# Optimization experiments

Hardware: AMD Instinct MI355X
Metric: run time of the kernel (lower is better)

The kernel has to match this reference:

```python
import jax, jax.numpy as jnp
import numpy as np

# (dv=3, dc=6)-regular Tanner graph: M checks, N=2M vars, E=M*dc edges
M, N, DV, DC, D, B, T = 1024, 2048, 3, 6, 8, 128, 5
CIN = DC * D          # check-MLP in/out dim = 48
VIN = DV * D + 1      # var-MLP in/out dim  = 25 (extra scalar = LLR)
HC, HV = 4 * CIN, 4 * VIN
EPS = 1e-6


def _graph():
    # variable j connects to checks (j + l) % M, l = 0..DV-1 -> every check has degree DC
    var_nbrs = (np.arange(N)[:, None] + np.arange(DV)[None, :]) % M   # [N, DV] check ids
    # var-edge id e = j*DV + l ; sort edges by check to get check-slot ordering
    order = np.argsort(var_nbrs.reshape(-1), kind='stable')           # check-edge p -> var-edge e
    chk_nbrs = (order // DV).reshape(M, DC)                           # var id in each check slot
    inv_order = np.argsort(order)                                     # var-edge e -> check-edge p
    return chk_nbrs, order, inv_order


def setup_inputs() -> dict:
    key = jax.random.key(0)
    ks = jax.random.split(key, 12)
    chk_nbrs, order, inv_order = _graph()
    prior = np.clip(np.random.default_rng(0).uniform(0.005, 0.05, size=N), EPS, 1 - EPS)
    prior_llr = jnp.asarray(np.log((1.0 - prior) / prior), jnp.float32)

    def lin_w(k, g, nin, nout):
        return jax.random.normal(k, (g, nin, nout), jnp.float32) / np.sqrt(nin)

    def lin_b(k, g, nout):
        return 0.02 * jax.random.normal(k, (g, nout), jnp.float32)

    return {
        "syndromes": jax.random.randint(ks[0], (B, M), 0, 2, jnp.int32),
        "prior_llr": prior_llr,
        "chk_w1": lin_w(ks[1], M, CIN, HC), "chk_b1": lin_b(ks[2], M, HC),
        "chk_w2": lin_w(ks[3], M, HC, CIN), "chk_b2": lin_b(ks[4], M, CIN),
        "var_w1": lin_w(ks[5], N, VIN, HV), "var_b1": lin_b(ks[6], N, HV),
        "var_w2": lin_w(ks[7], N, HV, VIN), "var_b2": lin_b(ks[8], N, VIN),
        "chk_nbrs": jnp.asarray(chk_nbrs, jnp.int32),      # [M, DC] var id per check slot
        "c2v_gather": jnp.asarray(inv_order, jnp.int32),   # var-edge -> check-edge perm
        "v2c_gather": jnp.asarray(order, jnp.int32),       # check-edge -> var-edge perm
    }


def reference(syndromes, prior_llr, chk_w1, chk_b1, chk_w2, chk_b2,
              var_w1, var_b1, var_w2, var_b2, chk_nbrs, c2v_gather, v2c_gather):
    synd_sgn = (1 - 2 * syndromes).astype(jnp.float32)                    # [B, M]
    prior_b = jnp.broadcast_to(prior_llr, (B, N))[..., None]              # [B, N, 1]

    def chk_mlp(x):  # x: [B, M, CIN], per-check grouped GEMM
        h = jax.nn.gelu(jnp.einsum('bmi,mih->bmh', x, chk_w1) + chk_b1, approximate=False)
        return jnp.einsum('bmh,mho->bmo', h, chk_w2) + chk_b2

    def var_mlp(x):  # x: [B, N, VIN]
        h = jax.nn.gelu(jnp.einsum('bni,nih->bnh', x, var_w1) + var_b1, approximate=False)
        return jnp.einsum('bnh,nho->bno', h, var_w2) + var_b2

    # init check in-messages: zeros with first component = prior LLR of neighbor var
    chk_in = jnp.zeros((B, M, DC, D), jnp.float32).at[..., 0].set(prior_llr[chk_nbrs][None])

    def step(chk_in, _):
        y = chk_mlp(chk_in.reshape(B, M, CIN)).reshape(B, M, DC, D)
        y = y * synd_sgn[:, :, None, None]                                # syndrome sign flip
        var_in = y.reshape(B, M * DC, D)[:, c2v_gather]                   # scatter c->v as gather
        x = jnp.concatenate([var_in.reshape(B, N, DV * D), prior_b], axis=-1)
        out = var_mlp(x)
        llr = out[..., DV * D]                                            # [B, N]
        msg = out[..., :DV * D].reshape(B, N * DV, D)
        chk_in_new = msg[:, v2c_gather].reshape(B, M, DC, D)              # scatter v->c as gather
        return chk_in_new, llr

    _, llrs = jax.lax.scan(step, chk_in, None, length=T)
    return llrs  # [T, B, N]
```

## Files before the change

kernel.cpp:

```cpp
#include <hip/hip_runtime.h>
#include <math.h>

#define MM 1024
#define NN 2048
#define BB 128
#define TT 5
#define EE 6144

typedef __bf16 bf16x8 __attribute__((ext_vector_type(8)));
typedef __bf16 bf16x4 __attribute__((ext_vector_type(4)));
typedef short  s16x4  __attribute__((ext_vector_type(4)));
typedef float  f32x4  __attribute__((ext_vector_type(4)));
typedef unsigned int u32x4 __attribute__((ext_vector_type(4)));

typedef const __attribute__((address_space(1))) void* gas_p;
typedef __attribute__((address_space(3))) void* las_p;

#define CHK_W_ELEMS 22272
#define CHK_L2_OFF  12288
#define VAR_W_ELEMS 7168
#define VAR_L2_OFF  3584

__device__ __forceinline__ float gelu_fast(float x) {
    float xe = x * 0.70710678118654752f;
    float ax = fabsf(xe);
    float t  = __builtin_amdgcn_rcpf(1.0f + 0.3275911f * ax);
    float p  = t * (0.254829592f + t * (-0.284496736f + t * (1.421413741f +
               t * (-1.453152027f + t * 1.061405429f))));
    float er = 1.0f - p * __expf(-xe * xe);
    er = copysignf(er, xe);
    return 0.5f * x * (1.0f + er);
}

__device__ __forceinline__ f32x4 mfma16(bf16x4 a, bf16x4 b, f32x4 c) {
#if __has_builtin(__builtin_amdgcn_mfma_f32_16x16x16bf16_1k)
    return __builtin_amdgcn_mfma_f32_16x16x16bf16_1k(
        __builtin_bit_cast(s16x4, a), __builtin_bit_cast(s16x4, b), c, 0, 0, 0);
#else
    f32x4 d;
    asm volatile("v_mfma_f32_16x16x16_bf16 %0, %1, %2, %3\n\ts_nop 4"
                 : "=v"(d) : "v"(a), "v"(b), "v"(c));
    return d;
#endif
}

__device__ __forceinline__ void wave_lds_fence() {
    asm volatile("s_waitcnt lgkmcnt(0)" ::: "memory");
}

__global__ __launch_bounds__(256, 6)
void prep_chk(const float* __restrict__ cw1, const float* __restrict__ cb1,
              const float* __restrict__ cw2, const float* __restrict__ cb2,
              __bf16* __restrict__ wchk)
{
    const int tid = threadIdx.x;
    const int w = tid >> 6, l = tid & 63, q = l >> 4, c = l & 15;

    __shared__ __align__(16) float s[6656];
    float* sw = s + w * 1664;

    const int m = blockIdx.x;
    const float* w1p = cw1 + (size_t)m * 9216;
    const float* w2p = cw2 + (size_t)m * 9216;
    __bf16* dst = wchk + (size_t)m * CHK_W_ELEMS;

    #pragma unroll
    for (int i0 = 0; i0 < 6; ++i0) {
        int i = i0 * 64 + l;
        int r = i / 12, c4 = i % 12;
        float4 v = *(const float4*)(w1p + r * 192 + w * 48 + c4 * 4);
        *(float2*)(sw + r * 50 + c4 * 4)     = make_float2(v.x, v.y);
        *(float2*)(sw + r * 50 + c4 * 4 + 2) = make_float2(v.z, v.w);
    }
    wave_lds_fence();
    #pragma unroll
    for (int d = 0; d < 3; ++d) {
        int mt = 3 * w + d;
        bf16x8 v;
        #pragma unroll
        for (int j = 0; j < 8; ++j)
            v[j] = (__bf16)sw[(q * 8 + j) * 50 + d * 16 + c];
        *(bf16x8*)(dst + (mt * 2) * 512 + l * 8) = v;
    }
    wave_lds_fence();

    #pragma unroll
    for (int i0 = 0; i0 < 4; ++i0) {
        int i = i0 * 64 + l;
        if (i < 204) {
            int r = i / 12, c4 = i % 12;
            const float* src = (r < 16)
                ? (w1p + (32 + r) * 192 + w * 48 + c4 * 4)
                : (cb1 + (size_t)m * 192 + w * 48 + c4 * 4);
            float4 v = *(const float4*)src;
            *(float2*)(sw + r * 50 + c4 * 4)     = make_float2(v.x, v.y);
            *(float2*)(sw + r * 50 + c4 * 4 + 2) = make_float2(v.z, v.w);
        }
    }
    wave_lds_fence();
    #pragma unroll
    for (int d = 0; d < 3; ++d) {
        int mt = 3 * w + d;
        bf16x8 v;
        #pragma unroll
        for (int j = 0; j < 8; ++j) {
            int lr = q * 8 + j;
            float wv = sw[lr * 50 + d * 16 + c];
            v[j] = (__bf16)((lr <= 16) ? wv : 0.0f);
        }
        *(bf16x8*)(dst + (mt * 2 + 1) * 512 + l * 8) = v;
    }
    wave_lds_fence();

    for (int t = w; t < 10; t += 4) {
        if (t < 9) {
            const int kb = t / 3, mt = t - kb * 3;
            #pragma unroll
            for (int i0 = 0; i0 < 4; ++i0) {
                int i = i0 * 64 + l;
                int r = i >> 2, c4 = i & 3;
                float4 v = *(const float4*)(w2p + (kb * 64 + r) * 48 + mt * 16 + c4 * 4);
                *(float4*)(sw + r * 20 + c4 * 4) = v;
            }
            wave_lds_fence();
            #pragma unroll
            for (int kk = 0; kk < 4; ++kk) {
                const int ks = kb * 4 + kk;
                const int kp = ks >> 1, half = ks & 1;
                bf16x4 v;
                #pragma unroll
                for (int r = 0; r < 4; ++r)
                    v[r] = (__bf16)sw[(kk * 16 + q * 4 + r) * 20 + c];
                *(bf16x4*)(dst + CHK_L2_OFF + mt * 3328 + kp * 512 + l * 8 + half * 4) = v;
            }
            wave_lds_fence();
        } else {
            #pragma unroll
            for (int mt = 0; mt < 3; ++mt) {
                bf16x4 v;
                #pragma unroll
                for (int r = 0; r < 4; ++r) v[r] = (__bf16)0.0f;
                if (q == 0) v[0] = (__bf16)cb2[(size_t)m * 48 + mt * 16 + c];
                *(bf16x4*)(dst + CHK_L2_OFF + mt * 3328 + 3072 + l * 4) = v;
            }
        }
    }
}

#define PREP_OTHER_GRID (2048 + 512 + 3072)

__global__ __launch_bounds__(256, 6)
void prep_other(const float* __restrict__ vw1, const float* __restrict__ vb1,
                const float* __restrict__ vw2, const float* __restrict__ vb2,
                const int* __restrict__ synd, const float* __restrict__ prior,
                __bf16* __restrict__ wvar, float* __restrict__ sgnT,
                __bf16* __restrict__ v2c)
{
    const int bid = blockIdx.x;
    const int tid = threadIdx.x;
    const int w = tid >> 6, l = tid & 63, q = l >> 4, c = l & 15;

    __shared__ __align__(16) float s[6656];
    float* sw = s + w * 1664;

    if (bid < 2048) {
        const int nv = bid;
        const float* w1p = vw1 + (size_t)nv * 2500;
        const float* w2p = vw2 + (size_t)nv * 2500;
        __bf16* dst = wvar + (size_t)nv * VAR_W_ELEMS;

        if (w < 3) {
            #pragma unroll
            for (int i0 = 0; i0 < 4; ++i0) {
                int i = i0 * 64 + l;
                if (i < 208) {
                    int r = i >> 3, c4 = i & 7;
                    const float* src = (r < 25)
                        ? (w1p + r * 100 + w * 32 + c4 * 4)
                        : (vb1 + (size_t)nv * 100 + w * 32 + c4 * 4);
                    float4 v = *(const float4*)src;
                    *(float2*)(sw + r * 34 + c4 * 4)     = make_float2(v.x, v.y);
                    *(float2*)(sw + r * 34 + c4 * 4 + 2) = make_float2(v.z, v.w);
                }
            }
        } else {
            if (l < 26) {
                int r = l;
                const float* src = (r < 25) ? (w1p + r * 100 + 96)
                                            : (vb1 + (size_t)nv * 100 + 96);
                float4 v = *(const float4*)src;
                *(float2*)(sw + r * 34)     = make_float2(v.x, v.y);
                *(float2*)(sw + r * 34 + 2) = make_float2(v.z, v.w);
            }
        }
        wave_lds_fence();
        {
            const int nmt = (w < 3) ? 2 : 1;
            #pragma unroll
            for (int d = 0; d < 2; ++d) {
                if (d < nmt) {
                    const int mt = (w < 3) ? (2 * w + d) : 6;
                    const int h = mt * 16 + c;
                    bf16x8 v;
                    #pragma unroll
                    for (int j = 0; j < 8; ++j) {
                        int k = q * 8 + j;
                        float wv = sw[k * 34 + d * 16 + c];
                        v[j] = (__bf16)((h < 100 && k <= 25) ? wv : 0.0f);
                    }
                    *(bf16x8*)(dst + mt * 512 + l * 8) = v;
                }
            }
        }
        wave_lds_fence();

        if (w < 3) {
            #pragma unroll
            for (int i0 = 0; i0 < 4; ++i0) {
                int i = i0 * 64 + l;
                if (i < 200)
                    *(float4*)(sw + i * 4) = *(const float4*)(w2p + 800 * w + i * 4);
            }
        } else {
            if (l < 25) *(float4*)(sw + l * 4) = *(const float4*)(w2p + 2400 + l * 4);
            if (l < 25) sw[100 + l] = vb2[(size_t)nv * 25 + l];
        }
        wave_lds_fence();
        {
            const int nks = (w < 3) ? 2 : 1;
            #pragma unroll
            for (int kk = 0; kk < 2; ++kk) {
                if (kk < nks) {
                    #pragma unroll
                    for (int mt = 0; mt < 2; ++mt) {
                        const int o = mt * 16 + c;
                        bf16x4 v;
                        #pragma unroll
                        for (int r = 0; r < 4; ++r) {
                            float x;
                            if (w < 3) {
                                int lk = kk * 16 + q * 4 + r;
                                float wv = sw[lk * 25 + o];
                                x = (o < 25) ? wv : 0.0f;
                            } else {
                                int lk = q * 4 + r;
                                float wv = sw[lk * 25 + o];
                                x = (o < 25 && lk <= 4) ? wv : 0.0f;
                            }
                            v[r] = (__bf16)x;
                        }
                        if (w < 3)
                            *(bf16x4*)(dst + VAR_L2_OFF + mt * 1792 + w * 512 + l * 8 + kk * 4) = v;
                        else
                            *(bf16x4*)(dst + VAR_L2_OFF + mt * 1792 + 1536 + l * 4) = v;
                    }
                }
            }
        }
    } else if (bid < 2560) {
        int idx = (bid - 2048) * 256 + tid;
        int m = idx >> 7, b = idx & 127;
        sgnT[idx] = (float)(1 - 2 * synd[(size_t)b * MM + m]);
    } else {
        int idx = (bid - 2560) * 256 + tid;
        int e = idx >> 7;
        bf16x8 v;
        #pragma unroll
        for (int j = 0; j < 8; ++j) v[j] = (__bf16)0.0f;
        v[0] = (__bf16)prior[e / 3];
        *(bf16x8*)(v2c + (size_t)idx * 8) = v;
    }
}

__device__ __forceinline__ void chk_layer1(const __bf16* wlds, int l,
                                           bf16x8 b0, bf16x8 b1, f32x4* acc)
{
    #pragma unroll
    for (int mt = 0; mt < 12; ++mt) {
        bf16x8 a0 = *(const bf16x8*)(wlds + (mt * 2 + 0) * 512 + l * 8);
        bf16x8 a1 = *(const bf16x8*)(wlds + (mt * 2 + 1) * 512 + l * 8);
        f32x4 z = {0.f, 0.f, 0.f, 0.f};
        z = __builtin_amdgcn_mfma_f32_16x16x32_bf16(a0, b0, z, 0, 0, 0);
        z = __builtin_amdgcn_mfma_f32_16x16x32_bf16(a1, b1, z, 0, 0, 0);
        acc[mt] = z;
    }
}

__device__ __forceinline__ void chk_layer2(const __bf16* wlds, int l, int q,
                                           const f32x4* acc, f32x4* acc2)
{
    #pragma unroll
    for (int mt = 0; mt < 3; ++mt) acc2[mt] = (f32x4){0.f, 0.f, 0.f, 0.f};
    #pragma unroll
    for (int kp = 0; kp < 6; ++kp) {
        bf16x4 bf0, bf1;
        #pragma unroll
        for (int r = 0; r < 4; ++r) bf0[r] = (__bf16)gelu_fast(acc[2 * kp][r]);
        #pragma unroll
        for (int r = 0; r < 4; ++r) bf1[r] = (__bf16)gelu_fast(acc[2 * kp + 1][r]);
        #pragma unroll
        for (int mt = 0; mt < 3; ++mt) {
            bf16x8 a8 = *(const bf16x8*)(wlds + CHK_L2_OFF + mt * 3328 + kp * 512 + l * 8);
            bf16x4 alo = {a8[0], a8[1], a8[2], a8[3]};
            bf16x4 ahi = {a8[4], a8[5], a8[6], a8[7]};
            acc2[mt] = mfma16(alo, bf0, acc2[mt]);
            acc2[mt] = mfma16(ahi, bf1, acc2[mt]);
        }
    }
    bf16x4 bfb;
    #pragma unroll
    for (int r = 0; r < 4; ++r) bfb[r] = (__bf16)0.0f;
    if (q == 0) bfb[0] = (__bf16)1.0f;
    #pragma unroll
    for (int mt = 0; mt < 3; ++mt) {
        bf16x4 af = *(const bf16x4*)(wlds + CHK_L2_OFF + mt * 3328 + 3072 + l * 4);
        acc2[mt] = mfma16(af, bfb, acc2[mt]);
    }
}

#define CPITCH 58
__global__ __launch_bounds__(256, 3)
void chk_kernel(const __bf16* __restrict__ wchk,
                const float* __restrict__ sgnT,
                const int* __restrict__ v2c_gather,
                const __bf16* __restrict__ v2c, __bf16* __restrict__ c2v)
{
    const int m = blockIdx.x;
    const int tid = threadIdx.x;
    const int w = tid >> 6, l = tid & 63, q = l >> 4, c = l & 15;

    __shared__ __align__(16) __bf16 wlds[CHK_W_ELEMS];
    __shared__ __align__(16) __bf16 ytile[4 * 16 * CPITCH];

    const int e0 = v2c_gather[m * 6 + q];
    const int e1 = (q < 2) ? v2c_gather[m * 6 + 4 + q] : 0;

    bf16x8 bA[2], bB[2];
    float sg[2];
    #pragma unroll
    for (int t2 = 0; t2 < 2; ++t2) {
        const int bt = t2 * 64 + w * 16;
        bA[t2] = *(const bf16x8*)(v2c + ((size_t)e0 * BB + bt + c) * 8);
        bf16x8 bb;
        #pragma unroll
        for (int j = 0; j < 8; ++j) bb[j] = (__bf16)0.0f;
        if (q < 2)       bb = *(const bf16x8*)(v2c + ((size_t)e1 * BB + bt + c) * 8);
        else if (q == 2) bb[0] = (__bf16)1.0f;
        bB[t2] = bb;
        sg[t2] = sgnT[m * BB + bt + c];
    }

    {
        const __bf16* src = wchk + (size_t)m * CHK_W_ELEMS;
        #pragma unroll
        for (int r = 0; r < 10; ++r)
            __builtin_amdgcn_global_load_lds(
                (gas_p)(src + (r * 256 + tid) * 8),
                (las_p)(wlds + (r * 256 + tid) * 8), 16, 0, 0);
        if (tid < 224)
            __builtin_amdgcn_global_load_lds(
                (gas_p)(src + (2560 + tid) * 8),
                (las_p)(wlds + (2560 + tid) * 8), 16, 0, 0);
    }
    __builtin_amdgcn_sched_barrier(0);
    asm volatile("s_waitcnt vmcnt(5)" ::: "memory");
    __syncthreads();

    __bf16* myy = ytile + w * 16 * CPITCH;

    f32x4 acc[12];
    chk_layer1(wlds, l, bA[0], bB[0], acc);

    __builtin_amdgcn_sched_barrier(0);
    asm volatile("s_waitcnt vmcnt(0)" ::: "memory");
    __syncthreads();

    #pragma unroll
    for (int t2 = 0; t2 < 2; ++t2) {
        if (t2 == 1) chk_layer1(wlds, l, bA[1], bB[1], acc);
        const int bt = t2 * 64 + w * 16;

        f32x4 acc2[3];
        chk_layer2(wlds, l, q, acc, acc2);

        #pragma unroll
        for (int mt = 0; mt < 3; ++mt)
            #pragma unroll
            for (int r = 0; r < 4; ++r)
                myy[c * CPITCH + mt * 16 + q * 4 + r] = (__bf16)(acc2[mt][r] * sg[t2]);
        wave_lds_fence();

        {
            int s = l >> 4, row = l & 15;
            u32x4 vv = *(const u32x4*)(myy + row * CPITCH + s * 8);
            *(u32x4*)(c2v + ((size_t)(m * 6 + s) * BB + bt + row) * 8) = vv;
            if (l < 32) {
                int s2 = 4 + (l >> 4), row2 = l & 15;
                u32x4 v2 = *(const u32x4*)(myy + row2 * CPITCH + s2 * 8);
                *(u32x4*)(c2v + ((size_t)(m * 6 + s2) * BB + bt + row2) * 8) = v2;
            }
        }
        wave_lds_fence();
    }
}

#define VPITCH 26
__global__ __launch_bounds__(256, 5)
void var_kernel(const __bf16* __restrict__ wvar,
                const int* __restrict__ c2v_gather, const float* __restrict__ prior,
                const __bf16* __restrict__ c2v, __bf16* __restrict__ v2c,
                float* __restrict__ llr_out, int last)
{
    const int nv = blockIdx.x;
    const int tid = threadIdx.x;
    const int w = tid >> 6, l = tid & 63, q = l >> 4, c = l & 15;

    __shared__ __align__(16) __bf16 wlds[VAR_W_ELEMS];
    __shared__ __align__(16) __bf16 ytile[4 * 16 * VPITCH];

    const int ep = (q < 3) ? c2v_gather[nv * 3 + q] : 0;
    const __bf16 prbf = (__bf16)prior[nv];

    bf16x8 bp[2];
    #pragma unroll
    for (int t2 = 0; t2 < 2; ++t2) {
        const int bt = t2 * 64 + w * 16;
        bf16x8 bb;
        #pragma unroll
        for (int j = 0; j < 8; ++j) bb[j] = (__bf16)0.0f;
        if (q < 3) bb = *(const bf16x8*)(c2v + ((size_t)ep * BB + bt + c) * 8);
        else { bb[0] = prbf; bb[1] = (__bf16)1.0f; }
        bp[t2] = bb;
    }

    {
        const __bf16* src = wvar + (size_t)nv * VAR_W_ELEMS;
        #pragma unroll
        for (int r = 0; r < 3; ++r)
            __builtin_amdgcn_global_load_lds(
                (gas_p)(src + (r * 256 + tid) * 8),
                (las_p)(wlds + (r * 256 + tid) * 8), 16, 0, 0);
        if (tid < 128)
            __builtin_amdgcn_global_load_lds(
                (gas_p)(src + (768 + tid) * 8),
                (las_p)(wlds + (768 + tid) * 8), 16, 0, 0);
    }
    __builtin_amdgcn_sched_barrier(0);
    asm volatile("s_waitcnt vmcnt(0)" ::: "memory");
    __syncthreads();

    __bf16* myy = ytile + w * 16 * VPITCH;

    #pragma unroll
    for (int t2 = 0; t2 < 2; ++t2) {
        const int bt = t2 * 64 + w * 16;
        const bf16x8 b0 = bp[t2];

        f32x4 acc[7];
        #pragma unroll
        for (int mt = 0; mt < 7; ++mt) {
            bf16x8 a0 = *(const bf16x8*)(wlds + mt * 512 + l * 8);
            f32x4 z = {0.f, 0.f, 0.f, 0.f};
            acc[mt] = __builtin_amdgcn_mfma_f32_16x16x32_bf16(a0, b0, z, 0, 0, 0);
        }

        f32x4 acc2[2];
        acc2[0] = (f32x4){0.f, 0.f, 0.f, 0.f};
        acc2[1] = (f32x4){0.f, 0.f, 0.f, 0.f};
        #pragma unroll
        for (int kp = 0; kp < 3; ++kp) {
            bf16x4 bf0, bf1;
            #pragma unroll
            for (int r = 0; r < 4; ++r) bf0[r] = (__bf16)gelu_fast(acc[2 * kp][r]);
            #pragma unroll
            for (int r = 0; r < 4; ++r) bf1[r] = (__bf16)gelu_fast(acc[2 * kp + 1][r]);
            #pragma unroll
            for (int mt = 0; mt < 2; ++mt) {
                bf16x8 a8 = *(const bf16x8*)(wlds + VAR_L2_OFF + mt * 1792 + kp * 512 + l * 8);
                bf16x4 alo = {a8[0], a8[1], a8[2], a8[3]};
                bf16x4 ahi = {a8[4], a8[5], a8[6], a8[7]};
                acc2[mt] = mfma16(alo, bf0, acc2[mt]);
                acc2[mt] = mfma16(ahi, bf1, acc2[mt]);
            }
        }
        {
            bf16x4 bf6;
            #pragma unroll
            for (int r = 0; r < 4; ++r) bf6[r] = (__bf16)gelu_fast(acc[6][r]);
            if (q == 1) bf6[0] = (__bf16)1.0f;
            #pragma unroll
            for (int mt = 0; mt < 2; ++mt) {
                bf16x4 af = *(const bf16x4*)(wlds + VAR_L2_OFF + mt * 1792 + 1536 + l * 4);
                acc2[mt] = mfma16(af, bf6, acc2[mt]);
            }
        }

        #pragma unroll
        for (int r = 0; r < 4; ++r)
            myy[c * VPITCH + q * 4 + r] = (__bf16)acc2[0][r];
        if (q < 2)
            #pragma unroll
            for (int r = 0; r < 4; ++r)
                myy[c * VPITCH + 16 + q * 4 + r] = (__bf16)acc2[1][r];
        if (q == 2) llr_out[(size_t)(bt + c) * NN + nv] = acc2[1][0];
        wave_lds_fence();

        if (!last && l < 48) {
            int s = l >> 4, row = l & 15;
            u32x4 vv = *(const u32x4*)(myy + row * VPITCH + s * 8);
            *(u32x4*)(v2c + ((size_t)(nv * 3 + s) * BB + bt + row) * 8) = vv;
        }
        wave_lds_fence();
    }
}

extern "C" void kernel_launch(void* const* d_in, const int* in_sizes, int n_in,
                              void* d_out, int out_size, void* d_ws, size_t ws_size,
                              hipStream_t stream) {
    const int*   syndromes = (const int*)  d_in[0];
    const float* prior_llr = (const float*)d_in[1];
    const float* chk_w1    = (const float*)d_in[2];
    const float* chk_b1    = (const float*)d_in[3];
    const float* chk_w2    = (const float*)d_in[4];
    const float* chk_b2    = (const float*)d_in[5];
    const float* var_w1    = (const float*)d_in[6];
    const float* var_b1    = (const float*)d_in[7];
    const float* var_w2    = (const float*)d_in[8];
    const float* var_b2    = (const float*)d_in[9];
    const int*   c2v_g     = (const int*)  d_in[11];
    const int*   v2c_g     = (const int*)  d_in[12];

    float* out = (float*)d_out;

    __bf16* v2c  = (__bf16*)d_ws;
    __bf16* c2v  = v2c + (size_t)EE * BB * 8;
    __bf16* wchk = c2v + (size_t)EE * BB * 8;
    __bf16* wvar = wchk + (size_t)MM * CHK_W_ELEMS;
    float*  sgnT = (float*)(wvar + (size_t)NN * VAR_W_ELEMS);

    prep_chk<<<MM, 256, 0, stream>>>(chk_w1, chk_b1, chk_w2, chk_b2, wchk);
    prep_other<<<PREP_OTHER_GRID, 256, 0, stream>>>(var_w1, var_b1, var_w2, var_b2,
                                                    syndromes, prior_llr,
                                                    wvar, sgnT, v2c);

    for (int t = 0; t < TT; ++t) {
        chk_kernel<<<MM, 256, 0, stream>>>(wchk, sgnT, v2c_g, v2c, c2v);
        var_kernel<<<NN, 256, 0, stream>>>(wvar, c2v_g, prior_llr, c2v, v2c,
                                           out + (size_t)t * BB * NN,
                                           (t == TT - 1) ? 1 : 0);
    }
}
```

Measured before the change: 394.9 us.

## Fuse check/variable iterations into one persistent cooperative kernel with grid sync

Replaces the ten alternating chk/var kernel launches with a single cooperative launch of 512 blocks. Each block processes 2 checks, then 4 variables per iteration, with grid.sync between stages. Variable weights are double-buffered in LDS so the next variable's weights load while the current one computes. This removes launch gaps but lowers parallelism from 1024/2048 blocks to 512. It also adds grid-barrier cost and serialises per-block work, which may expose the weight-load latency.

```diff
diff --git a/kernel.cpp b/kernel.cpp
--- a/kernel.cpp
+++ b/kernel.cpp
@@ -1,5 +1,8 @@
 #include <hip/hip_runtime.h>
+#include <hip/hip_cooperative_groups.h>
 #include <math.h>
+
+namespace cg = cooperative_groups;
 
 #define MM 1024
 #define NN 2048
@@ -319,19 +322,14 @@
 }
 
 #define CPITCH 58
-__global__ __launch_bounds__(256, 3)
-void chk_kernel(const __bf16* __restrict__ wchk,
-                const float* __restrict__ sgnT,
-                const int* __restrict__ v2c_gather,
-                const __bf16* __restrict__ v2c, __bf16* __restrict__ c2v)
-{
-    const int m = blockIdx.x;
-    const int tid = threadIdx.x;
-    const int w = tid >> 6, l = tid & 63, q = l >> 4, c = l & 15;
-
-    __shared__ __align__(16) __bf16 wlds[CHK_W_ELEMS];
-    __shared__ __align__(16) __bf16 ytile[4 * 16 * CPITCH];
-
+#define VPITCH 26
+
+__device__ __forceinline__ void chk_task(
+    int m, int tid, int w, int l, int q, int c,
+    const __bf16* __restrict__ wchk, const float* __restrict__ sgnT,
+    const int* __restrict__ v2c_gather, const __bf16* __restrict__ v2c,
+    __bf16* __restrict__ c2v, __bf16* wlds, __bf16* myy)
+{
     const int e0 = v2c_gather[m * 6 + q];
     const int e1 = (q < 2) ? v2c_gather[m * 6 + 4 + q] : 0;
 
@@ -366,8 +364,6 @@
     asm volatile("s_waitcnt vmcnt(5)" ::: "memory");
     __syncthreads();
 
-    __bf16* myy = ytile + w * 16 * CPITCH;
-
     f32x4 acc[12];
     chk_layer1(wlds, l, bA[0], bB[0], acc);
 
@@ -402,9 +398,177 @@
         }
         wave_lds_fence();
     }
-}
-
-#define VPITCH 26
+    __syncthreads();
+}
+
+__device__ __forceinline__ void var_stage(const __bf16* __restrict__ wvar,
+                                          int nv, int tid, __bf16* buf)
+{
+    const __bf16* src = wvar + (size_t)nv * VAR_W_ELEMS;
+    #pragma unroll
+    for (int r = 0; r < 3; ++r)
+        __builtin_amdgcn_global_load_lds(
+            (gas_p)(src + (r * 256 + tid) * 8),
+            (las_p)(buf + (r * 256 + tid) * 8), 16, 0, 0);
+    if (tid < 128)
+        __builtin_amdgcn_global_load_lds(
+            (gas_p)(src + (768 + tid) * 8),
+            (las_p)(buf + (768 + tid) * 8), 16, 0, 0);
+}
+
+__global__ __launch_bounds__(256, 3)
+void loop_kernel(const __bf16* __restrict__ wchk, const __bf16* __restrict__ wvar,
+                 const float* __restrict__ sgnT,
+                 const int* __restrict__ v2c_gather, const int* __restrict__ c2v_gather,
+                 const float* __restrict__ prior,
+                 __bf16* __restrict__ v2c, __bf16* __restrict__ c2v,
+                 float* __restrict__ out)
+{
+    cg::grid_group grid = cg::this_grid();
+    const int bid = blockIdx.x;
+    const int tid = threadIdx.x;
+    const int w = tid >> 6, l = tid & 63, q = l >> 4, c = l & 15;
+
+    __shared__ __align__(16) __bf16 wlds[CHK_W_ELEMS];
+    __shared__ __align__(16) __bf16 ytile[4 * 16 * CPITCH];
+
+    __bf16* wv0 = wlds;
+    __bf16* wv1 = wlds + VAR_W_ELEMS;
+    __bf16* myyC = ytile + w * 16 * CPITCH;
+    __bf16* myyV = ytile + w * 16 * VPITCH;
+
+    for (int t = 0; t < TT; ++t) {
+        #pragma unroll 1
+        for (int i = 0; i < 2; ++i)
+            chk_task(bid * 2 + i, tid, w, l, q, c,
+                     wchk, sgnT, v2c_gather, v2c, c2v, wlds, myyC);
+
+        __threadfence();
+        grid.sync();
+
+        const int last = (t == TT - 1);
+        int eps[4];
+        float prs[4];
+        #pragma unroll
+        for (int jj = 0; jj < 4; ++jj) {
+            int nvq = bid * 4 + jj;
+            eps[jj] = (q < 3) ? c2v_gather[nvq * 3 + q] : 0;
+            prs[jj] = prior[nvq];
+        }
+
+        var_stage(wvar, bid * 4, tid, wv0);
+
+        #pragma unroll
+        for (int j = 0; j < 4; ++j) {
+            const int nv = bid * 4 + j;
+            __bf16* buf = (j & 1) ? wv1 : wv0;
+
+            __builtin_amdgcn_sched_barrier(0);
+            asm volatile("s_waitcnt vmcnt(0)" ::: "memory");
+            __syncthreads();
+
+            bf16x8 bp[2];
+            #pragma unroll
+            for (int t2 = 0; t2 < 2; ++t2) {
+                const int bt = t2 * 64 + w * 16;
+                bf16x8 bb;
+                #pragma unroll
+                for (int jj = 0; jj < 8; ++jj) bb[jj] = (__bf16)0.0f;
+                if (q < 3) bb = *(const bf16x8*)(c2v + ((size_t)eps[j] * BB + bt + c) * 8);
+                else { bb[0] = (__bf16)prs[j]; bb[1] = (__bf16)1.0f; }
+                bp[t2] = bb;
+            }
+            __builtin_amdgcn_sched_barrier(0);
+            if (j < 3) var_stage(wvar, nv + 1, tid, (j & 1) ? wv0 : wv1);
+
+            #pragma unroll
+            for (int t2 = 0; t2 < 2; ++t2) {
+                const int bt = t2 * 64 + w * 16;
+                const bf16x8 b0 = bp[t2];
+
+                f32x4 acc[7];
+                #pragma unroll
+                for (int mt = 0; mt < 7; ++mt) {
+                    bf16x8 a0 = *(const bf16x8*)(buf + mt * 512 + l * 8);
+                    f32x4 z = {0.f, 0.f, 0.f, 0.f};
+                    acc[mt] = __builtin_amdgcn_mfma_f32_16x16x32_bf16(a0, b0, z, 0, 0, 0);
+                }
+
+                f32x4 acc2[2];
+                acc2[0] = (f32x4){0.f, 0.f, 0.f, 0.f};
+                acc2[1] = (f32x4){0.f, 0.f, 0.f, 0.f};
+                #pragma unroll
+                for (int kp = 0; kp < 3; ++kp) {
+                    bf16x4 bf0, bf1;
+                    #pragma unroll
+                    for (int r = 0; r < 4; ++r) bf0[r] = (__bf16)gelu_fast(acc[2 * kp][r]);
+                    #pragma unroll
+                    for (int r = 0; r < 4; ++r) bf1[r] = (__bf16)gelu_fast(acc[2 * kp + 1][r]);
+                    #pragma unroll
+                    for (int mt = 0; mt < 2; ++mt) {
+                        bf16x8 a8 = *(const bf16x8*)(buf + VAR_L2_OFF + mt * 1792 + kp * 512 + l * 8);
+                        bf16x4 alo = {a8[0], a8[1], a8[2], a8[3]};
+                        bf16x4 ahi = {a8[4], a8[5], a8[6], a8[7]};
+                        acc2[mt] = mfma16(alo, bf0, acc2[mt]);
+                        acc2[mt] = mfma16(ahi, bf1, acc2[mt]);
+                    }
+                }
+                {
+                    bf16x4 bf6;
+                    #pragma unroll
+                    for (int r = 0; r < 4; ++r) bf6[r] = (__bf16)gelu_fast(acc[6][r]);
+                    if (q == 1) bf6[0] = (__bf16)1.0f;
+                    #pragma unroll
+                    for (int mt = 0; mt < 2; ++mt) {
+                        bf16x4 af = *(const bf16x4*)(buf + VAR_L2_OFF + mt * 1792 + 1536 + l * 4);
+                        acc2[mt] = mfma16(af, bf6, acc2[mt]);
+                    }
+                }
+
+                #pragma unroll
+                for (int r = 0; r < 4; ++r)
+                    myyV[c * VPITCH + q * 4 + r] = (__bf16)acc2[0][r];
+                if (q < 2)
+                    #pragma unroll
+                    for (int r = 0; r < 4; ++r)
+                        myyV[c * VPITCH + 16 + q * 4 + r] = (__bf16)acc2[1][r];
+                if (q == 2) out[(size_t)t * BB * NN + (size_t)(bt + c) * NN + nv] = acc2[1][0];
+                wave_lds_fence();
+
+                if (!last && l < 48) {
+                    int s = l >> 4, row = l & 15;
+                    u32x4 vv = *(const u32x4*)(myyV + row * VPITCH + s * 8);
+                    *(u32x4*)(v2c + ((size_t)(nv * 3 + s) * BB + bt + row) * 8) = vv;
+                }
+                wave_lds_fence();
+            }
+        }
+        __syncthreads();
+
+        if (t != TT - 1) {
+            __threadfence();
+            grid.sync();
+        }
+    }
+}
+
+__global__ __launch_bounds__(256, 3)
+void chk_kernel(const __bf16* __restrict__ wchk,
+                const float* __restrict__ sgnT,
+                const int* __restrict__ v2c_gather,
+                const __bf16* __restrict__ v2c, __bf16* __restrict__ c2v)
+{
+    const int m = blockIdx.x;
+    const int tid = threadIdx.x;
+    const int w = tid >> 6, l = tid & 63, q = l >> 4, c = l & 15;
+
+    __shared__ __align__(16) __bf16 wlds[CHK_W_ELEMS];
+    __shared__ __align__(16) __bf16 ytile[4 * 16 * CPITCH];
+
+    chk_task(m, tid, w, l, q, c, wchk, sgnT, v2c_gather, v2c, c2v,
+             wlds, ytile + w * 16 * CPITCH);
+}
+
 __global__ __launch_bounds__(256, 5)
 void var_kernel(const __bf16* __restrict__ wvar,
                 const int* __restrict__ c2v_gather, const float* __restrict__ prior,
@@ -433,18 +597,7 @@
         bp[t2] = bb;
     }
 
-    {
-        const __bf16* src = wvar + (size_t)nv * VAR_W_ELEMS;
-        #pragma unroll
-        for (int r = 0; r < 3; ++r)
-            __builtin_amdgcn_global_load_lds(
-                (gas_p)(src + (r * 256 + tid) * 8),
-                (las_p)(wlds + (r * 256 + tid) * 8), 16, 0, 0);
-        if (tid < 128)
-            __builtin_amdgcn_global_load_lds(
-                (gas_p)(src + (768 + tid) * 8),
-                (las_p)(wlds + (768 + tid) * 8), 16, 0, 0);
-    }
+    var_stage(wvar, nv, tid, wlds);
     __builtin_amdgcn_sched_barrier(0);
     asm volatile("s_waitcnt vmcnt(0)" ::: "memory");
     __syncthreads();
@@ -543,10 +696,21 @@
                                                     syndromes, prior_llr,
                                                     wvar, sgnT, v2c);
 
-    for (int t = 0; t < TT; ++t) {
-        chk_kernel<<<MM, 256, 0, stream>>>(wchk, sgnT, v2c_g, v2c, c2v);
-        var_kernel<<<NN, 256, 0, stream>>>(wvar, c2v_g, prior_llr, c2v, v2c,
-                                           out + (size_t)t * BB * NN,
-                                           (t == TT - 1) ? 1 : 0);
-    }
-}
+    const __bf16* wchk_c = wchk; const __bf16* wvar_c = wvar;
+    const float* sgnT_c = sgnT;
+    void* kargs[] = {(void*)&wchk_c, (void*)&wvar_c, (void*)&sgnT_c,
+                     (void*)&v2c_g, (void*)&c2v_g, (void*)&prior_llr,
+                     (void*)&v2c, (void*)&c2v, (void*)&out};
+    hipError_t err = hipLaunchCooperativeKernel(
+        reinterpret_cast<const void*>(loop_kernel),
+        dim3(512), dim3(256), kargs, 0, stream);
+
+    if (err != hipSuccess) {
+        for (int t = 0; t < TT; ++t) {
+            chk_kernel<<<MM, 256, 0, stream>>>(wchk, sgnT, v2c_g, v2c, c2v);
+            var_kernel<<<NN, 256, 0, stream>>>(wvar, c2v_g, prior_llr, c2v, v2c,
+                                               out + (size_t)t * BB * NN,
+                                               (t == TT - 1) ? 1 : 0);
+        }
+    }
+}
```

Measured after the change: 1.348 ms. 241% more time.

## Stream check layer-2 weights from global and pipeline two variables per var block

Applied to the files above, without the earlier changes.

In the check kernel, only the layer-1 weights are staged in LDS. Layer-2 weights are read straight from global memory, which shrinks LDS use so occupancy can rise from 3 to 4 blocks per CU. The variable kernel now handles two variable nodes per block, issuing the second node's weight load into a separate LDS buffer while the first node computes, so the load latency is overlapped. The costs are uncached-by-LDS global reads inside the check layer-2 loop, the loss of the earlier layer-1 overlap in the check kernel, and lower var-kernel occupancy (launch bound 5 to 4) with half as many blocks.

```diff
diff --git a/kernel.cpp b/kernel.cpp
--- a/kernel.cpp
+++ b/kernel.cpp
@@ -18,6 +18,7 @@
 
 #define CHK_W_ELEMS 22272
 #define CHK_L2_OFF  12288
+#define CHK_L1_ELEMS 12288
 #define VAR_W_ELEMS 7168
 #define VAR_L2_OFF  3584
 
@@ -286,8 +287,9 @@
     }
 }
 
-__device__ __forceinline__ void chk_layer2(const __bf16* wlds, int l, int q,
-                                           const f32x4* acc, f32x4* acc2)
+__device__ __forceinline__ void chk_layer2g(const __bf16* __restrict__ wl2,
+                                            int l, int q,
+                                            const f32x4* acc, f32x4* acc2)
 {
     #pragma unroll
     for (int mt = 0; mt < 3; ++mt) acc2[mt] = (f32x4){0.f, 0.f, 0.f, 0.f};
@@ -300,7 +302,7 @@
         for (int r = 0; r < 4; ++r) bf1[r] = (__bf16)gelu_fast(acc[2 * kp + 1][r]);
         #pragma unroll
         for (int mt = 0; mt < 3; ++mt) {
-            bf16x8 a8 = *(const bf16x8*)(wlds + CHK_L2_OFF + mt * 3328 + kp * 512 + l * 8);
+            bf16x8 a8 = *(const bf16x8*)(wl2 + mt * 3328 + kp * 512 + l * 8);
             bf16x4 alo = {a8[0], a8[1], a8[2], a8[3]};
             bf16x4 ahi = {a8[4], a8[5], a8[6], a8[7]};
             acc2[mt] = mfma16(alo, bf0, acc2[mt]);
@@ -313,13 +315,15 @@
     if (q == 0) bfb[0] = (__bf16)1.0f;
     #pragma unroll
     for (int mt = 0; mt < 3; ++mt) {
-        bf16x4 af = *(const bf16x4*)(wlds + CHK_L2_OFF + mt * 3328 + 3072 + l * 4);
+        bf16x4 af = *(const bf16x4*)(wl2 + mt * 3328 + 3072 + l * 4);
         acc2[mt] = mfma16(af, bfb, acc2[mt]);
     }
 }
 
 #define CPITCH 58
-__global__ __launch_bounds__(256, 3)
+#define VPITCH 26
+
+__global__ __launch_bounds__(256, 4)
 void chk_kernel(const __bf16* __restrict__ wchk,
                 const float* __restrict__ sgnT,
                 const int* __restrict__ v2c_gather,
@@ -329,8 +333,10 @@
     const int tid = threadIdx.x;
     const int w = tid >> 6, l = tid & 63, q = l >> 4, c = l & 15;
 
-    __shared__ __align__(16) __bf16 wlds[CHK_W_ELEMS];
+    __shared__ __align__(16) __bf16 wlds[CHK_L1_ELEMS];
     __shared__ __align__(16) __bf16 ytile[4 * 16 * CPITCH];
+
+    const __bf16* wl2 = wchk + (size_t)m * CHK_W_ELEMS + CHK_L2_OFF;
 
     const int e0 = v2c_gather[m * 6 + q];
     const int e1 = (q < 2) ? v2c_gather[m * 6 + 4 + q] : 0;
@@ -353,35 +359,26 @@
     {
         const __bf16* src = wchk + (size_t)m * CHK_W_ELEMS;
         #pragma unroll
-        for (int r = 0; r < 10; ++r)
+        for (int r = 0; r < 6; ++r)
             __builtin_amdgcn_global_load_lds(
                 (gas_p)(src + (r * 256 + tid) * 8),
                 (las_p)(wlds + (r * 256 + tid) * 8), 16, 0, 0);
-        if (tid < 224)
-            __builtin_amdgcn_global_load_lds(
-                (gas_p)(src + (2560 + tid) * 8),
-                (las_p)(wlds + (2560 + tid) * 8), 16, 0, 0);
-    }
-    __builtin_amdgcn_sched_barrier(0);
-    asm volatile("s_waitcnt vmcnt(5)" ::: "memory");
-    __syncthreads();
-
-    __bf16* myy = ytile + w * 16 * CPITCH;
-
-    f32x4 acc[12];
-    chk_layer1(wlds, l, bA[0], bB[0], acc);
-
+    }
     __builtin_amdgcn_sched_barrier(0);
     asm volatile("s_waitcnt vmcnt(0)" ::: "memory");
     __syncthreads();
 
+    __bf16* myy = ytile + w * 16 * CPITCH;
+
     #pragma unroll
     for (int t2 = 0; t2 < 2; ++t2) {
-        if (t2 == 1) chk_layer1(wlds, l, bA[1], bB[1], acc);
         const int bt = t2 * 64 + w * 16;
 
+        f32x4 acc[12];
+        chk_layer1(wlds, l, bA[t2], bB[t2], acc);
+
         f32x4 acc2[3];
-        chk_layer2(wlds, l, q, acc, acc2);
+        chk_layer2g(wl2, l, q, acc, acc2);
 
         #pragma unroll
         for (int mt = 0; mt < 3; ++mt)
@@ -404,114 +401,151 @@
     }
 }
 
-#define VPITCH 26
-__global__ __launch_bounds__(256, 5)
+__device__ __forceinline__ void var_stage4(const __bf16* __restrict__ wvar,
+                                           int nv, int tid, __bf16* buf)
+{
+    const __bf16* src = wvar + (size_t)nv * VAR_W_ELEMS;
+    #pragma unroll
+    for (int r = 0; r < 3; ++r)
+        __builtin_amdgcn_global_load_lds(
+            (gas_p)(src + (r * 256 + tid) * 8),
+            (las_p)(buf + (r * 256 + tid) * 8), 16, 0, 0);
+    if (tid < 128)
+        __builtin_amdgcn_global_load_lds(
+            (gas_p)(src + (768 + tid) * 8),
+            (las_p)(buf + (768 + tid) * 8), 16, 0, 0);
+}
+
+__device__ __forceinline__ void var_compute(
+    const __bf16* buf, const bf16x8* bp, int nv,
+    int w, int l, int q, int c, int last,
+    __bf16* myy, __bf16* __restrict__ v2c, float* __restrict__ llr_out)
+{
+    #pragma unroll
+    for (int t2 = 0; t2 < 2; ++t2) {
+        const int bt = t2 * 64 + w * 16;
+        const bf16x8 b0 = bp[t2];
+
+        f32x4 acc[7];
+        #pragma unroll
+        for (int mt = 0; mt < 7; ++mt) {
+            bf16x8 a0 = *(const bf16x8*)(buf + mt * 512 + l * 8);
+            f32x4 z = {0.f, 0.f, 0.f, 0.f};
+            acc[mt] = __builtin_amdgcn_mfma_f32_16x16x32_bf16(a0, b0, z, 0, 0, 0);
+        }
+
+        f32x4 acc2[2];
+        acc2[0] = (f32x4){0.f, 0.f, 0.f, 0.f};
+        acc2[1] = (f32x4){0.f, 0.f, 0.f, 0.f};
+        #pragma unroll
+        for (int kp = 0; kp < 3; ++kp) {
+            bf16x4 bf0, bf1;
+            #pragma unroll
+            for (int r = 0; r < 4; ++r) bf0[r] = (__bf16)gelu_fast(acc[2 * kp][r]);
+            #pragma unroll
+            for (int r = 0; r < 4; ++r) bf1[r] = (__bf16)gelu_fast(acc[2 * kp + 1][r]);
+            #pragma unroll
+            for (int mt = 0; mt < 2; ++mt) {
+                bf16x8 a8 = *(const bf16x8*)(buf + VAR_L2_OFF + mt * 1792 + kp * 512 + l * 8);
+                bf16x4 alo = {a8[0], a8[1], a8[2], a8[3]};
+                bf16x4 ahi = {a8[4], a8[5], a8[6], a8[7]};
+                acc2[mt] = mfma16(alo, bf0, acc2[mt]);
+                acc2[mt] = mfma16(ahi, bf1, acc2[mt]);
+            }
+        }
+        {
+            bf16x4 bf6;
+            #pragma unroll
+            for (int r = 0; r < 4; ++r) bf6[r] = (__bf16)gelu_fast(acc[6][r]);
+            if (q == 1) bf6[0] = (__bf16)1.0f;
+            #pragma unroll
+            for (int mt = 0; mt < 2; ++mt) {
+                bf16x4 af = *(const bf16x4*)(buf + VAR_L2_OFF + mt * 1792 + 1536 + l * 4);
+                acc2[mt] = mfma16(af, bf6, acc2[mt]);
+            }
+        }
+
+        #pragma unroll
+        for (int r = 0; r < 4; ++r)
+            myy[c * VPITCH + q * 4 + r] = (__bf16)acc2[0][r];
+        if (q < 2)
+            #pragma unroll
+            for (int r = 0; r < 4; ++r)
+                myy[c * VPITCH + 16 + q * 4 + r] = (__bf16)acc2[1][r];
+        if (q == 2) llr_out[(size_t)(bt + c) * NN + nv] = acc2[1][0];
+        wave_lds_fence();
+
+        if (!last && l < 48) {
+            int s = l >> 4, row = l & 15;
+            u32x4 vv = *(const u32x4*)(myy + row * VPITCH + s * 8);
+            *(u32x4*)(v2c + ((size_t)(nv * 3 + s) * BB + bt + row) * 8) = vv;
+        }
+        wave_lds_fence();
+    }
+}
+
+__global__ __launch_bounds__(256, 4)
 void var_kernel(const __bf16* __restrict__ wvar,
                 const int* __restrict__ c2v_gather, const float* __restrict__ prior,
                 const __bf16* __restrict__ c2v, __bf16* __restrict__ v2c,
                 float* __restrict__ llr_out, int last)
 {
-    const int nv = blockIdx.x;
+    const int nv0 = blockIdx.x * 2;
     const int tid = threadIdx.x;
     const int w = tid >> 6, l = tid & 63, q = l >> 4, c = l & 15;
 
-    __shared__ __align__(16) __bf16 wlds[VAR_W_ELEMS];
+    __shared__ __align__(16) __bf16 wbuf[2 * VAR_W_ELEMS];
     __shared__ __align__(16) __bf16 ytile[4 * 16 * VPITCH];
 
-    const int ep = (q < 3) ? c2v_gather[nv * 3 + q] : 0;
-    const __bf16 prbf = (__bf16)prior[nv];
-
-    bf16x8 bp[2];
+    int eps[2];
+    float prs[2];
+    #pragma unroll
+    for (int j = 0; j < 2; ++j) {
+        eps[j] = (q < 3) ? c2v_gather[(nv0 + j) * 3 + q] : 0;
+        prs[j] = prior[nv0 + j];
+    }
+
+    var_stage4(wvar, nv0, tid, wbuf);
+
+    bf16x8 bp0[2];
     #pragma unroll
     for (int t2 = 0; t2 < 2; ++t2) {
         const int bt = t2 * 64 + w * 16;
         bf16x8 bb;
         #pragma unroll
         for (int j = 0; j < 8; ++j) bb[j] = (__bf16)0.0f;
-        if (q < 3) bb = *(const bf16x8*)(c2v + ((size_t)ep * BB + bt + c) * 8);
-        else { bb[0] = prbf; bb[1] = (__bf16)1.0f; }
-        bp[t2] = bb;
-    }
-
-    {
-        const __bf16* src = wvar + (size_t)nv * VAR_W_ELEMS;
-        #pragma unroll
-        for (int r = 0; r < 3; ++r)
-            __builtin_amdgcn_global_load_lds(
-                (gas_p)(src + (r * 256 + tid) * 8),
-                (las_p)(wlds + (r * 256 + tid) * 8), 16, 0, 0);
-        if (tid < 128)
-            __builtin_amdgcn_global_load_lds(
-                (gas_p)(src + (768 + tid) * 8),
-                (las_p)(wlds + (768 + tid) * 8), 16, 0, 0);
+        if (q < 3) bb = *(const bf16x8*)(c2v + ((size_t)eps[0] * BB + bt + c) * 8);
+        else { bb[0] = (__bf16)prs[0]; bb[1] = (__bf16)1.0f; }
+        bp0[t2] = bb;
+    }
+    __builtin_amdgcn_sched_barrier(0);
+
+    var_stage4(wvar, nv0 + 1, tid, wbuf + VAR_W_ELEMS);
+    __builtin_amdgcn_sched_barrier(0);
+    asm volatile("s_waitcnt vmcnt(4)" ::: "memory");
+    __syncthreads();
+
+    __bf16* myy = ytile + w * 16 * VPITCH;
+
+    var_compute(wbuf, bp0, nv0, w, l, q, c, last, myy, v2c, llr_out);
+
+    bf16x8 bp1[2];
+    #pragma unroll
+    for (int t2 = 0; t2 < 2; ++t2) {
+        const int bt = t2 * 64 + w * 16;
+        bf16x8 bb;
+        #pragma unroll
+        for (int j = 0; j < 8; ++j) bb[j] = (__bf16)0.0f;
+        if (q < 3) bb = *(const bf16x8*)(c2v + ((size_t)eps[1] * BB + bt + c) * 8);
+        else { bb[0] = (__bf16)prs[1]; bb[1] = (__bf16)1.0f; }
+        bp1[t2] = bb;
     }
     __builtin_amdgcn_sched_barrier(0);
     asm volatile("s_waitcnt vmcnt(0)" ::: "memory");
     __syncthreads();
 
-    __bf16* myy = ytile + w * 16 * VPITCH;
-
-    #pragma unroll
-    for (int t2 = 0; t2 < 2; ++t2) {
-        const int bt = t2 * 64 + w * 16;
-        const bf16x8 b0 = bp[t2];
-
-        f32x4 acc[7];
-        #pragma unroll
-        for (int mt = 0; mt < 7; ++mt) {
-            bf16x8 a0 = *(const bf16x8*)(wlds + mt * 512 + l * 8);
-            f32x4 z = {0.f, 0.f, 0.f, 0.f};
-            acc[mt] = __builtin_amdgcn_mfma_f32_16x16x32_bf16(a0, b0, z, 0, 0, 0);
-        }
-
-        f32x4 acc2[2];
-        acc2[0] = (f32x4){0.f, 0.f, 0.f, 0.f};
-        acc2[1] = (f32x4){0.f, 0.f, 0.f, 0.f};
-        #pragma unroll
-        for (int kp = 0; kp < 3; ++kp) {
-            bf16x4 bf0, bf1;
-            #pragma unroll
-            for (int r = 0; r < 4; ++r) bf0[r] = (__bf16)gelu_fast(acc[2 * kp][r]);
-            #pragma unroll
-            for (int r = 0; r < 4; ++r) bf1[r] = (__bf16)gelu_fast(acc[2 * kp + 1][r]);
-            #pragma unroll
-            for (int mt = 0; mt < 2; ++mt) {
-                bf16x8 a8 = *(const bf16x8*)(wlds + VAR_L2_OFF + mt * 1792 + kp * 512 + l * 8);
-                bf16x4 alo = {a8[0], a8[1], a8[2], a8[3]};
-                bf16x4 ahi = {a8[4], a8[5], a8[6], a8[7]};
-                acc2[mt] = mfma16(alo, bf0, acc2[mt]);
-                acc2[mt] = mfma16(ahi, bf1, acc2[mt]);
-            }
-        }
-        {
-            bf16x4 bf6;
-            #pragma unroll
-            for (int r = 0; r < 4; ++r) bf6[r] = (__bf16)gelu_fast(acc[6][r]);
-            if (q == 1) bf6[0] = (__bf16)1.0f;
-            #pragma unroll
-            for (int mt = 0; mt < 2; ++mt) {
-                bf16x4 af = *(const bf16x4*)(wlds + VAR_L2_OFF + mt * 1792 + 1536 + l * 4);
-                acc2[mt] = mfma16(af, bf6, acc2[mt]);
-            }
-        }
-
-        #pragma unroll
-        for (int r = 0; r < 4; ++r)
-            myy[c * VPITCH + q * 4 + r] = (__bf16)acc2[0][r];
-        if (q < 2)
-            #pragma unroll
-            for (int r = 0; r < 4; ++r)
-                myy[c * VPITCH + 16 + q * 4 + r] = (__bf16)acc2[1][r];
-        if (q == 2) llr_out[(size_t)(bt + c) * NN + nv] = acc2[1][0];
-        wave_lds_fence();
-
-        if (!last && l < 48) {
-            int s = l >> 4, row = l & 15;
-            u32x4 vv = *(const u32x4*)(myy + row * VPITCH + s * 8);
-            *(u32x4*)(v2c + ((size_t)(nv * 3 + s) * BB + bt + row) * 8) = vv;
-        }
-        wave_lds_fence();
-    }
+    var_compute(wbuf + VAR_W_ELEMS, bp1, nv0 + 1, w, l, q, c, last,
+                myy, v2c, llr_out);
 }
 
 extern "C" void kernel_launch(void* const* d_in, const int* in_sizes, int n_in,
@@ -545,8 +579,8 @@
 
     for (int t = 0; t < TT; ++t) {
         chk_kernel<<<MM, 256, 0, stream>>>(wchk, sgnT, v2c_g, v2c, c2v);
-        var_kernel<<<NN, 256, 0, stream>>>(wvar, c2v_g, prior_llr, c2v, v2c,
-                                           out + (size_t)t * BB * NN,
-                                           (t == TT - 1) ? 1 : 0);
-    }
-}
+        var_kernel<<<NN / 2, 256, 0, stream>>>(wvar, c2v_g, prior_llr, c2v, v2c,
+                                               out + (size_t)t * BB * NN,
+                                               (t == TT - 1) ? 1 : 0);
+    }
+}
```

After: 443.4 us. +12.3%, slower.
